# Optimization experiments

Hardware: AMD Instinct MI355X
Metric: run time of the kernel (lower is better)

Reference implementation:

```python
import jax, jax.numpy as jnp
import numpy as np

B, P, C = 32, 8732, 21
TOP_K = 200
CONF_THRESH = 0.01
NMS_THRESH = 0.45
VAR0, VAR1 = 0.1, 0.2  # VOC PRIOR_BOX VARIANCE


def setup_inputs() -> dict:
    key = jax.random.key(0)
    k1, k2, k3 = jax.random.split(key, 3)
    loc_data = jax.random.normal(k1, (B, P, 4), jnp.float32)
    conf_data = jax.random.uniform(k2, (B, P, C), jnp.float32)
    prior_data = jax.random.uniform(k3, (P, 4), jnp.float32)
    return {"loc_data": loc_data, "conf_data": conf_data, "prior_data": prior_data}


def _decode(loc, priors):
    # priors are (cx, cy, w, h); returns (x1, y1, x2, y2)
    cxcy = priors[:, :2] + loc[:, :2] * VAR0 * priors[:, 2:]
    wh = priors[:, 2:] * jnp.exp(loc[:, 2:] * VAR1)
    x1y1 = cxcy - wh * 0.5
    return jnp.concatenate([x1y1, x1y1 + wh], axis=1)  # [P,4]


def _nms_class(boxes, scores):
    # boxes [P,4], scores [P] -> [TOP_K,5] rows of (score, x1, y1, x2, y2)
    s = jnp.where(scores > CONF_THRESH, scores, -1.0)
    top_s, idx = jax.lax.top_k(s, TOP_K)          # descending scores
    b = boxes[idx]                                 # [K,4]
    valid = top_s > CONF_THRESH
    x1, y1, x2, y2 = b[:, 0], b[:, 1], b[:, 2], b[:, 3]
    area = (x2 - x1) * (y2 - y1)
    # pairwise intersection / IoU [K,K]
    xx1 = jnp.maximum(x1[:, None], x1[None, :])
    yy1 = jnp.maximum(y1[:, None], y1[None, :])
    xx2 = jnp.minimum(x2[:, None], x2[None, :])
    yy2 = jnp.minimum(y2[:, None], y2[None, :])
    inter = jnp.clip(xx2 - xx1, 0.0) * jnp.clip(yy2 - yy1, 0.0)
    union = area[:, None] + area[None, :] - inter
    iou = inter / union
    ar = jnp.arange(TOP_K)

    def step(carry, j):
        kept, suppressed = carry
        is_kept = valid[j] & ~suppressed[j]
        kept = kept.at[j].set(is_kept)
        suppressed = suppressed | (is_kept & (iou[j] > NMS_THRESH) & (ar > j))
        return (kept, suppressed), None

    (kept, _), _ = jax.lax.scan(
        step, (jnp.zeros(TOP_K, bool), jnp.zeros(TOP_K, bool)), ar)
    # compact kept rows to the front (matches output[i, cl, :count] = ...)
    pos = jnp.cumsum(kept) - 1
    safe = jnp.where(kept, pos, TOP_K)
    rows = jnp.concatenate([top_s[:, None], b], axis=1)  # [K,5]
    out = jnp.zeros((TOP_K + 1, 5), rows.dtype).at[safe].set(rows)[:TOP_K]
    return out


def reference(loc_data, conf_data, prior_data):
    def per_image(loc, conf):
        boxes = _decode(loc, prior_data)           # [P,4]
        return jax.vmap(lambda s: _nms_class(boxes, s), in_axes=1)(conf)  # [C,K,5]

    out = jax.vmap(per_image)(loc_data, conf_data)  # [B,C,K,5]
    return out.at[:, 0].set(0.0)  # class 0 (background) is skipped in original
```

## Files before the change

### kernel.cpp

```cpp
#include <hip/hip_runtime.h>
#include <stdint.h>

#define B_ 32
#define P_ 8732
#define C_ 21
#define TOPK 200
#define TGT 228
#define TGT0 300
#define SUBCAP 28
#define NCH2 35
#define NSLOT (NCH2 * SUBCAP)
#define CONF_T 0.01f
#define NMS_T 0.45f
#define NT 512
#define KV4 5
#define NTASK (B_ * C_)

__device__ __forceinline__ uint32_t f2s(float f) {
    uint32_t u = __float_as_uint(f);
    return (u & 0x80000000u) ? ~u : (u | 0x80000000u);
}
__device__ __forceinline__ float s2f(uint32_t s) {
    uint32_t b = (s & 0x80000000u) ? (s & 0x7FFFFFFFu) : ~s;
    return __uint_as_float(b);
}
__device__ __forceinline__ uint32_t keyof(float v) {
    return f2s((v > CONF_T) ? v : -1.0f);
}
__device__ __forceinline__ uint32_t thr0() {
    return f2s(1.0f - (float)TGT0 / (float)P_);
}

__global__ __launch_bounds__(256) void scatter_cands(const float* __restrict__ conf,
                                                     uint32_t* __restrict__ gccnt,
                                                     uint64_t* __restrict__ gcand) {
    const int b = blockIdx.x / NCH2;
    const int ch = blockIdx.x % NCH2;
    const int p0 = ch * 256;
    const int n = min(256, P_ - p0);
    const int tid = threadIdx.x;
    const int lane = tid & 63;
    const int cs = tid >> 6;
    __shared__ float tile[256 * C_];
    const float4* src4 = (const float4*)(conf + ((size_t)b * P_ + p0) * C_);
    float4* tile4 = (float4*)tile;
    const int tot4 = (n * C_) >> 2;
    for (int i = tid; i < tot4; i += 256) tile4[i] = src4[i];
    __syncthreads();
    const uint32_t T0 = thr0();
    const bool act = (4 * lane) < n;
    for (int c = (cs == 0 ? 4 : cs); c < C_; c += 4) {
        uint32_t kk[4];
        int nq = 0;
        if (act) {
            const float* tp = &tile[4 * lane * C_ + c];
            kk[0] = keyof(tp[0 * C_]);
            kk[1] = keyof(tp[1 * C_]);
            kk[2] = keyof(tp[2 * C_]);
            kk[3] = keyof(tp[3 * C_]);
            nq = (kk[0] >= T0) + (kk[1] >= T0) + (kk[2] >= T0) + (kk[3] >= T0);
        }
        int incl = nq;
        #pragma unroll
        for (int d = 1; d < 64; d <<= 1) {
            int v = __shfl_up(incl, d);
            if (lane >= d) incl += v;
        }
        const int excl = incl - nq;
        const int total = __shfl(incl, 63);
        const int task = b * C_ + c;
        uint64_t* dst = gcand + ((size_t)task * NCH2 + ch) * SUBCAP;
        if (nq) {
            int pos = excl;
            const int pb = p0 + 4 * lane;
            #pragma unroll
            for (int k = 0; k < 4; ++k) {
                if (kk[k] >= T0) {
                    if (pos < SUBCAP)
                        dst[pos] = ((uint64_t)kk[k] << 32) | (uint32_t)(~(uint32_t)(pb + k));
                    ++pos;
                }
            }
        }
        if (lane == 0) gccnt[(size_t)task * NCH2 + ch] = (uint32_t)total;
    }
}

template<bool HASWS>
__global__ __launch_bounds__(NT, 6) void detect_kernel(
    const float* __restrict__ loc, const float* __restrict__ prior,
    const uint32_t* __restrict__ gccnt, const uint64_t* __restrict__ gcand,
    const float* __restrict__ conf, float* __restrict__ out)
{
    const int task = blockIdx.x;
    const int b = task / C_;
    const int c = task % C_;
    const int tid = threadIdx.x;
    const int lane = tid & 63;
    float* outp = out + (size_t)task * TOPK * 5;

    if (c == 0) {
        for (int e = tid; e < TOPK * 5; e += NT) outp[e] = 0.0f;
        return;
    }

    __shared__ uint64_t cand[256];
    __shared__ float4 bbox[TOPK];
    __shared__ float bs[TOPK];
    __shared__ unsigned long long msk[TOPK * 4];
    __shared__ unsigned long long vmask[4];
    __shared__ int order[TOPK];
    __shared__ int s_cnt, s_nk;
    __shared__ int s_c2[2];
    __shared__ uint32_t s_ccnt[NCH2];
    __shared__ int s_gc, s_bad;

    const uint32_t T0 = thr0();

    if (tid == 0) s_cnt = 0;
    if (tid < 2) s_c2[tid] = 0;
    if (HASWS && tid < NCH2) s_ccnt[tid] = gccnt[(size_t)task * NCH2 + tid];
    for (int i2 = tid; i2 < TOPK * 4; i2 += NT) msk[i2] = 0ull;
    __syncthreads();
    if (HASWS && tid < 64) {
        uint32_t cc = (lane < NCH2) ? s_ccnt[lane] : 0u;
        int bad = (cc > SUBCAP) ? 1 : 0;
        int tot = (int)cc;
        #pragma unroll
        for (int d = 1; d < 64; d <<= 1) {
            tot += __shfl_down(tot, d);
            bad |= __shfl_down(bad, d);
        }
        if (lane == 0) { s_gc = tot; s_bad = bad; }
    }
    __syncthreads();

    const bool fast = HASWS && !s_bad && s_gc >= TOPK;
    const int gc = HASWS ? s_gc : 0;

    uint64_t vc0 = 0, vc1 = 0;
    bool val0 = false, val1 = false;
    uint4 kv[KV4];
    if (fast) {
        const uint64_t* gp = gcand + (size_t)task * NSLOT;
        {
            const int ch0 = tid / SUBCAP, i0 = tid - ch0 * SUBCAP;
            if (i0 < (int)s_ccnt[ch0]) { vc0 = gp[tid]; val0 = true; }
        }
        const int s1 = tid + NT;
        if (s1 < NSLOT) {
            const int ch1 = s1 / SUBCAP, i1 = s1 - ch1 * SUBCAP;
            if (i1 < (int)s_ccnt[ch1]) { vc1 = gp[s1]; val1 = true; }
        }
    } else {
        const float* sp = conf + (size_t)b * P_ * C_ + c;
        #pragma unroll
        for (int r = 0; r < KV4; ++r) {
            uint32_t uu[4];
            #pragma unroll
            for (int c4 = 0; c4 < 4; ++c4) {
                int p = (tid + r * NT) * 4 + c4;
                if (p < P_) {
                    float v = sp[(size_t)p * C_];
                    v = (v > CONF_T) ? v : -1.0f;
                    uu[c4] = f2s(v);
                } else uu[c4] = 0u;
            }
            kv[r] = make_uint4(uu[0], uu[1], uu[2], uu[3]);
        }
    }

    if (fast) {
        uint32_t vthr = T0;
        if (gc > 256) {
            const uint32_t k0 = (uint32_t)(vc0 >> 32);
            const uint32_t k1 = (uint32_t)(vc1 >> 32);
            uint32_t lo = T0, hi = 0xFFFFFFFFu;
            uint32_t t;
            {
                const float sc = s2f(T0);
                const float sn = 1.0f - (1.0f - sc) * (float)TGT / (float)gc;
                t = f2s(sn);
                if (!(t > lo && t < hi)) t = lo + ((hi - lo) >> 1);
            }
            for (int it = 0; ; ++it) {
                const int slot = it & 1;
                int my = (val0 && k0 >= t) + (val1 && k1 >= t);
                #pragma unroll
                for (int d = 1; d < 64; d <<= 1) my += __shfl_down(my, d);
                if (lane == 0) atomicAdd(&s_c2[slot], my);
                __syncthreads();
                const int cnt = s_c2[slot];
                __syncthreads();
                if (tid == 0) s_c2[slot] = 0;
                if (cnt >= TOPK && cnt <= 256) { vthr = t; break; }
                if (cnt > 256) lo = t; else hi = t;
                if (hi - lo <= 1) { vthr = lo; break; }
                uint32_t tn = 0;
                bool bis = (it >= 8) || (cnt == 0);
                if (!bis) {
                    const float sc = s2f(t);
                    const float sn = 1.0f - (1.0f - sc) * (float)TGT / (float)cnt;
                    tn = f2s(sn);
                    if (!(tn > lo && tn < hi)) bis = true;
                }
                if (bis) tn = lo + ((hi - lo) >> 1);
                t = tn;
            }
        }
        if (val0 && (uint32_t)(vc0 >> 32) >= vthr) {
            int pos = atomicAdd(&s_cnt, 1);
            if (pos < 256) cand[pos] = vc0;
        }
        if (val1 && (uint32_t)(vc1 >> 32) >= vthr) {
            int pos = atomicAdd(&s_cnt, 1);
            if (pos < 256) cand[pos] = vc1;
        }
    } else {
        uint32_t lo = 0u, hi = 0xFFFFFFFFu;
        uint32_t t = f2s(1.0f - (float)TGT / (float)P_);
        uint32_t vthr = 0u;
        for (int it = 0; ; ++it) {
            const int slot = it & 1;
            int my = 0;
            #pragma unroll
            for (int r = 0; r < KV4; ++r)
                my += (kv[r].x >= t) + (kv[r].y >= t) + (kv[r].z >= t) + (kv[r].w >= t);
            #pragma unroll
            for (int d = 1; d < 64; d <<= 1) my += __shfl_down(my, d);
            if (lane == 0) atomicAdd(&s_c2[slot], my);
            __syncthreads();
            const int cnt = s_c2[slot];
            __syncthreads();
            if (tid == 0) s_c2[slot] = 0;
            if (cnt >= TOPK && cnt <= 256) { vthr = t; break; }
            if (cnt > 256) lo = t; else hi = t;
            if (hi - lo <= 1) { vthr = lo; break; }
            uint32_t tn = 0;
            bool bis = (it >= 8) || (cnt == 0);
            if (!bis) {
                const float sc = s2f(t);
                const float sn = 1.0f - (1.0f - sc) * (float)TGT / (float)cnt;
                tn = f2s(sn);
                if (!(tn > lo && tn < hi)) bis = true;
            }
            if (bis) tn = lo + ((hi - lo) >> 1);
            t = tn;
        }
        #pragma unroll
        for (int r = 0; r < KV4; ++r) {
            const int pb = (tid + r * NT) * 4;
            uint32_t uu[4] = {kv[r].x, kv[r].y, kv[r].z, kv[r].w};
            #pragma unroll
            for (int c4 = 0; c4 < 4; ++c4) {
                uint32_t u = uu[c4];
                if (u >= vthr) {
                    int pos = atomicAdd(&s_cnt, 1);
                    if (pos < 256) cand[pos] = ((uint64_t)u << 32) | (uint32_t)(~(uint32_t)(pb + c4));
                }
            }
        }
    }
    __syncthreads();
    if (tid < 256 && tid >= s_cnt) cand[tid] = 0ull;
    __syncthreads();

    uint64_t v = (tid < 256) ? cand[tid] : 0ull;
    for (int kk = 2; kk <= 256; kk <<= 1) {
        for (int j = kk >> 1; j > 0; j >>= 1) {
            if (j >= 64) {
                __syncthreads();
                if (tid < 256) cand[tid] = v;
                __syncthreads();
                if (tid < 256) {
                    uint64_t pv = cand[tid ^ j];
                    bool keepmax = (((tid & j) == 0) == ((tid & kk) == 0));
                    v = keepmax ? (v > pv ? v : pv) : (v < pv ? v : pv);
                }
            } else if (tid < 256) {
                uint64_t pv = __shfl_xor(v, j);
                bool keepmax = (((tid & j) == 0) == ((tid & kk) == 0));
                v = keepmax ? (v > pv ? v : pv) : (v < pv ? v : pv);
            }
        }
    }

    float my_sc = -1.0f;
    if (tid < TOPK) {
        uint32_t su = (uint32_t)(v >> 32);
        int p = (int)(~(uint32_t)v);
        my_sc = s2f(su);
        const float4 l4 = *(const float4*)(loc + ((size_t)b * P_ + p) * 4);
        const float4 pr = *(const float4*)(prior + (size_t)p * 4);
        float cx = __fadd_rn(pr.x, __fmul_rn(__fmul_rn(l4.x, 0.1f), pr.z));
        float cy = __fadd_rn(pr.y, __fmul_rn(__fmul_rn(l4.y, 0.1f), pr.w));
        float ew = (float)exp((double)__fmul_rn(l4.z, 0.2f));
        float eh = (float)exp((double)__fmul_rn(l4.w, 0.2f));
        float w  = __fmul_rn(pr.z, ew);
        float h  = __fmul_rn(pr.w, eh);
        float x1 = __fsub_rn(cx, __fmul_rn(w, 0.5f));
        float y1 = __fsub_rn(cy, __fmul_rn(h, 0.5f));
        float x2 = __fadd_rn(x1, w);
        float y2 = __fadd_rn(y1, h);
        bs[tid] = my_sc;
        bbox[tid] = make_float4(x1, y1, x2, y2);
    }
    {
        unsigned long long bm = __ballot(tid < TOPK && my_sc > CONF_T);
        if (lane == 0 && tid < 256) vmask[tid >> 6] = bm;
    }
    __syncthreads();

    if (tid < 500) {
        const int rp = tid / 5;
        const int s  = tid - rp * 5;
        #pragma unroll
        for (int pass = 0; pass < 2; ++pass) {
            const int j  = pass ? (199 - rp) : rp;
            const int i0 = j + 1 + s;
            const float4 bj = bbox[j];
            const float  aj = __fmul_rn(__fsub_rn(bj.z, bj.x), __fsub_rn(bj.w, bj.y));
            for (int i = i0; i < TOPK; i += 5) {
                const float4 bi = bbox[i];
                float xx1 = fmaxf(bj.x, bi.x);
                float yy1 = fmaxf(bj.y, bi.y);
                float xx2 = fminf(bj.z, bi.z);
                float yy2 = fminf(bj.w, bi.w);
                float dx = fmaxf(__fsub_rn(xx2, xx1), 0.0f);
                float dy = fmaxf(__fsub_rn(yy2, yy1), 0.0f);
                float inter = __fmul_rn(dx, dy);
                if (inter > 0.0f) {
                    float ai = __fmul_rn(__fsub_rn(bi.z, bi.x), __fsub_rn(bi.w, bi.y));
                    float uni = __fsub_rn(__fadd_rn(aj, ai), inter);
                    float t45 = __fmul_rn(NMS_T, uni);
                    float mar = __fmul_rn(t45, 1e-6f);
                    bool sup;
                    if (inter > __fadd_rn(t45, mar)) sup = true;
                    else if (inter < __fsub_rn(t45, mar)) sup = false;
                    else sup = (inter / uni > NMS_T);
                    if (sup) atomicOr(&msk[j * 4 + (i >> 6)], 1ull << (i & 63));
                }
            }
        }
    }
    __syncthreads();

    if (tid < 64) {
        const int L = tid;
        auto or_reduce = [&](unsigned long long x) {
            #pragma unroll
            for (int d = 1; d < 64; d <<= 1) x |= __shfl_xor(x, d);
            return x;
        };
        unsigned long long s1 = 0, s2 = 0, s3 = 0;
        int nk = 0;
        #pragma unroll
        for (int w = 0; w < 4; ++w) {
            const int j = (w << 6) | L;
            unsigned long long r0 = 0, r1 = 0, r2 = 0, r3 = 0;
            if (j < TOPK) {
                const unsigned long long* mr = &msk[j * 4];
                r0 = mr[0]; r1 = mr[1]; r2 = mr[2]; r3 = mr[3];
            }
            const unsigned long long rself = (w == 0) ? r0 : (w == 1) ? r1
                                           : (w == 2) ? r2 : r3;
            unsigned long long sw = (w == 0) ? 0ull : (w == 1) ? s1
                                  : (w == 2) ? s2 : s3;
            unsigned long long alive = vmask[w] & ~sw;
            unsigned long long pm = 0;
            while (alive) {
                int jl = __ffsll(alive) - 1;
                if (L == 0) order[nk] = (w << 6) | jl;
                ++nk;
                sw |= __shfl(rself, jl);
                pm |= (1ull << jl);
                alive &= ~(sw | (1ull << jl));
            }
            if (pm) {
                const bool picked = (pm >> L) & 1ull;
                if (w == 0) {
                    s1 |= or_reduce(picked ? r1 : 0ull);
                    s2 |= or_reduce(picked ? r2 : 0ull);
                    s3 |= or_reduce(picked ? r3 : 0ull);
                } else if (w == 1) {
                    s2 |= or_reduce(picked ? r2 : 0ull);
                    s3 |= or_reduce(picked ? r3 : 0ull);
                } else if (w == 2) {
                    s3 |= or_reduce(picked ? r3 : 0ull);
                }
            }
        }
        if (L == 0) s_nk = nk;
    }
    __syncthreads();

    const int nk = s_nk;
    for (int e = tid; e < TOPK * 5; e += NT) {
        int r = e / 5;
        int f = e - r * 5;
        float val = 0.0f;
        if (r < nk) {
            int j = order[r];
            float4 bb = bbox[j];
            val = (f == 0) ? bs[j] : (f == 1) ? bb.x : (f == 2) ? bb.y
                : (f == 3) ? bb.z : bb.w;
        }
        outp[e] = val;
    }
}

extern "C" void kernel_launch(void* const* d_in, const int* in_sizes, int n_in,
                              void* d_out, int out_size, void* d_ws, size_t ws_size,
                              hipStream_t stream) {
    const float* loc   = (const float*)d_in[0];
    const float* conf  = (const float*)d_in[1];
    const float* prior = (const float*)d_in[2];
    float* out = (float*)d_out;

    const size_t cnt_bytes  = (size_t)NTASK * NCH2 * sizeof(uint32_t);
    const size_t cand_bytes = (size_t)NTASK * NSLOT * sizeof(uint64_t);
    if (ws_size >= cnt_bytes + cand_bytes) {
        uint32_t* gccnt = (uint32_t*)d_ws;
        uint64_t* gcand = (uint64_t*)((char*)d_ws + cnt_bytes);
        scatter_cands<<<B_ * NCH2, 256, 0, stream>>>(conf, gccnt, gcand);
        detect_kernel<true><<<NTASK, NT, 0, stream>>>(loc, prior, gccnt, gcand, conf, out);
    } else {
        detect_kernel<false><<<NTASK, NT, 0, stream>>>(loc, prior, nullptr, nullptr, conf, out);
    }
}
```

Baseline: 123.3 us.

## Pack four NMS tasks per block and use ballot compaction in scatter

The detect kernel now runs four (image, class) tasks per 1024-thread block, each with 256 threads, instead of one task per 512-thread block. Shared arrays are indexed per task, and the threshold search loop is made block-uniform through a shared active flag. Background-class tasks no longer exit early; they run the common path with work masked off. The IoU pairwise work is redistributed over 200 threads. The scatter kernel replaces its 4-per-lane shuffle prefix scan with a ballot/popcount compaction over 64-point groups. Risks: the four tasks share every barrier, so each waits for the slowest one's search iterations, and a block now needs four times the shared memory.

```diff
diff --git a/kernel.cpp b/kernel.cpp
--- a/kernel.cpp
+++ b/kernel.cpp
@@ -12,9 +12,12 @@
 #define NSLOT (NCH2 * SUBCAP)
 #define CONF_T 0.01f
 #define NMS_T 0.45f
-#define NT 512
-#define KV4 5
 #define NTASK (B_ * C_)
+#define GT 4
+#define HT 256
+#define NTB (GT * HT)
+#define NBLK (NTASK / GT)
+#define KV4H 9
 
 __device__ __forceinline__ uint32_t f2s(float f) {
     uint32_t u = __float_as_uint(f);
@@ -40,7 +43,7 @@
     const int n = min(256, P_ - p0);
     const int tid = threadIdx.x;
     const int lane = tid & 63;
-    const int cs = tid >> 6;
+    const int wv = tid >> 6;
     __shared__ float tile[256 * C_];
     const float4* src4 = (const float4*)(conf + ((size_t)b * P_ + p0) * C_);
     float4* tile4 = (float4*)tile;
@@ -48,82 +51,66 @@
     for (int i = tid; i < tot4; i += 256) tile4[i] = src4[i];
     __syncthreads();
     const uint32_t T0 = thr0();
-    const bool act = (4 * lane) < n;
-    for (int c = (cs == 0 ? 4 : cs); c < C_; c += 4) {
-        uint32_t kk[4];
-        int nq = 0;
-        if (act) {
-            const float* tp = &tile[4 * lane * C_ + c];
-            kk[0] = keyof(tp[0 * C_]);
-            kk[1] = keyof(tp[1 * C_]);
-            kk[2] = keyof(tp[2 * C_]);
-            kk[3] = keyof(tp[3 * C_]);
-            nq = (kk[0] >= T0) + (kk[1] >= T0) + (kk[2] >= T0) + (kk[3] >= T0);
-        }
-        int incl = nq;
-        #pragma unroll
-        for (int d = 1; d < 64; d <<= 1) {
-            int v = __shfl_up(incl, d);
-            if (lane >= d) incl += v;
-        }
-        const int excl = incl - nq;
-        const int total = __shfl(incl, 63);
-        const int task = b * C_ + c;
-        uint64_t* dst = gcand + ((size_t)task * NCH2 + ch) * SUBCAP;
-        if (nq) {
-            int pos = excl;
-            const int pb = p0 + 4 * lane;
-            #pragma unroll
-            for (int k = 0; k < 4; ++k) {
-                if (kk[k] >= T0) {
-                    if (pos < SUBCAP)
-                        dst[pos] = ((uint64_t)kk[k] << 32) | (uint32_t)(~(uint32_t)(pb + k));
-                    ++pos;
-                }
-            }
-        }
-        if (lane == 0) gccnt[(size_t)task * NCH2 + ch] = (uint32_t)total;
+    const unsigned long long lmask = (1ull << lane) - 1ull;
+    for (int c = (wv == 0 ? 4 : wv); c < C_; c += 4) {
+        int base = 0;
+        uint64_t* dst = gcand + ((size_t)(b * C_ + c) * NCH2 + ch) * SUBCAP;
+        #pragma unroll
+        for (int itp = 0; itp < 4; ++itp) {
+            const int p = itp * 64 + lane;
+            bool q = false; uint32_t key = 0;
+            if (p < n) {
+                key = keyof(tile[p * C_ + c]);
+                q = (key >= T0);
+            }
+            const unsigned long long bm = __ballot(q);
+            if (q) {
+                int pos = base + (int)__popcll(bm & lmask);
+                if (pos < SUBCAP)
+                    dst[pos] = ((uint64_t)key << 32) | (uint32_t)(~(uint32_t)(p0 + p));
+            }
+            base += (int)__popcll(bm);
+        }
+        if (lane == 0) gccnt[(size_t)(b * C_ + c) * NCH2 + ch] = (uint32_t)base;
     }
 }
 
 template<bool HASWS>
-__global__ __launch_bounds__(NT, 6) void detect_kernel(
+__global__ __launch_bounds__(NTB, 4) void detect_kernel(
     const float* __restrict__ loc, const float* __restrict__ prior,
     const uint32_t* __restrict__ gccnt, const uint64_t* __restrict__ gcand,
     const float* __restrict__ conf, float* __restrict__ out)
 {
-    const int task = blockIdx.x;
+    const int tid = threadIdx.x;
+    const int h   = tid >> 8;
+    const int ht  = tid & 255;
+    const int lane = tid & 63;
+    const int task = blockIdx.x * GT + h;
     const int b = task / C_;
     const int c = task % C_;
-    const int tid = threadIdx.x;
-    const int lane = tid & 63;
+    const bool live = (c != 0);
     float* outp = out + (size_t)task * TOPK * 5;
 
-    if (c == 0) {
-        for (int e = tid; e < TOPK * 5; e += NT) outp[e] = 0.0f;
-        return;
-    }
-
-    __shared__ uint64_t cand[256];
-    __shared__ float4 bbox[TOPK];
-    __shared__ float bs[TOPK];
-    __shared__ unsigned long long msk[TOPK * 4];
-    __shared__ unsigned long long vmask[4];
-    __shared__ int order[TOPK];
-    __shared__ int s_cnt, s_nk;
-    __shared__ int s_c2[2];
-    __shared__ uint32_t s_ccnt[NCH2];
-    __shared__ int s_gc, s_bad;
+    __shared__ uint64_t cand[GT][256];
+    __shared__ float4 bbox[GT][TOPK];
+    __shared__ float bs[GT][TOPK];
+    __shared__ unsigned long long msk[GT][TOPK * 4];
+    __shared__ unsigned long long vmask[GT][4];
+    __shared__ int order[GT][TOPK];
+    __shared__ int s_cnt[GT], s_nk[GT];
+    __shared__ int s_c2[GT][2];
+    __shared__ uint32_t s_ccnt[GT][NCH2];
+    __shared__ int s_gc[GT], s_bad[GT], s_act[GT];
 
     const uint32_t T0 = thr0();
 
-    if (tid == 0) s_cnt = 0;
-    if (tid < 2) s_c2[tid] = 0;
-    if (HASWS && tid < NCH2) s_ccnt[tid] = gccnt[(size_t)task * NCH2 + tid];
-    for (int i2 = tid; i2 < TOPK * 4; i2 += NT) msk[i2] = 0ull;
-    __syncthreads();
-    if (HASWS && tid < 64) {
-        uint32_t cc = (lane < NCH2) ? s_ccnt[lane] : 0u;
+    if (ht == 0) s_cnt[h] = 0;
+    if (ht < 2) s_c2[h][ht] = 0;
+    if (HASWS && ht < NCH2) s_ccnt[h][ht] = gccnt[(size_t)task * NCH2 + ht];
+    for (int i = ht; i < TOPK * 4; i += HT) msk[h][i] = 0ull;
+    __syncthreads();
+    if (HASWS && ht < 64) {
+        uint32_t cc = (lane < NCH2) ? s_ccnt[h][lane] : 0u;
         int bad = (cc > SUBCAP) ? 1 : 0;
         int tot = (int)cc;
         #pragma unroll
@@ -131,162 +118,156 @@
             tot += __shfl_down(tot, d);
             bad |= __shfl_down(bad, d);
         }
-        if (lane == 0) { s_gc = tot; s_bad = bad; }
-    }
-    __syncthreads();
-
-    const bool fast = HASWS && !s_bad && s_gc >= TOPK;
-    const int gc = HASWS ? s_gc : 0;
-
-    uint64_t vc0 = 0, vc1 = 0;
-    bool val0 = false, val1 = false;
-    uint4 kv[KV4];
+        if (lane == 0) { s_gc[h] = tot; s_bad[h] = bad; }
+    }
+    __syncthreads();
+
+    const bool fast = HASWS && live && !s_bad[h] && s_gc[h] >= TOPK;
+    const int gc = fast ? s_gc[h] : 0;
+
+    uint64_t vc[4] = {0, 0, 0, 0};
+    bool val[4] = {false, false, false, false};
+    uint4 kv[KV4H];
+    #pragma unroll
+    for (int r = 0; r < KV4H; ++r) kv[r] = make_uint4(0u, 0u, 0u, 0u);
     if (fast) {
         const uint64_t* gp = gcand + (size_t)task * NSLOT;
-        {
-            const int ch0 = tid / SUBCAP, i0 = tid - ch0 * SUBCAP;
-            if (i0 < (int)s_ccnt[ch0]) { vc0 = gp[tid]; val0 = true; }
-        }
-        const int s1 = tid + NT;
-        if (s1 < NSLOT) {
-            const int ch1 = s1 / SUBCAP, i1 = s1 - ch1 * SUBCAP;
-            if (i1 < (int)s_ccnt[ch1]) { vc1 = gp[s1]; val1 = true; }
-        }
-    } else {
+        #pragma unroll
+        for (int k = 0; k < 4; ++k) {
+            const int s = ht + k * HT;
+            if (s < NSLOT) {
+                const int chh = s / SUBCAP, ii = s - chh * SUBCAP;
+                if (ii < (int)s_ccnt[h][chh]) { vc[k] = gp[s]; val[k] = true; }
+            }
+        }
+    } else if (live) {
         const float* sp = conf + (size_t)b * P_ * C_ + c;
         #pragma unroll
-        for (int r = 0; r < KV4; ++r) {
+        for (int r = 0; r < KV4H; ++r) {
             uint32_t uu[4];
             #pragma unroll
-            for (int c4 = 0; c4 < 4; ++c4) {
-                int p = (tid + r * NT) * 4 + c4;
-                if (p < P_) {
-                    float v = sp[(size_t)p * C_];
-                    v = (v > CONF_T) ? v : -1.0f;
-                    uu[c4] = f2s(v);
-                } else uu[c4] = 0u;
+            for (int q = 0; q < 4; ++q) {
+                const int p = (ht + r * HT) * 4 + q;
+                uu[q] = (p < P_) ? keyof(sp[(size_t)p * C_]) : 0u;
             }
             kv[r] = make_uint4(uu[0], uu[1], uu[2], uu[3]);
         }
     }
 
-    if (fast) {
-        uint32_t vthr = T0;
+    bool active = false;
+    uint32_t t = 0, lo = 0, hi = 0xFFFFFFFFu, vthr = 0;
+    int it2 = 0;
+    if (!live) {
+        vthr = 0xFFFFFFFFu;
+    } else if (fast) {
+        lo = T0; vthr = T0;
         if (gc > 256) {
-            const uint32_t k0 = (uint32_t)(vc0 >> 32);
-            const uint32_t k1 = (uint32_t)(vc1 >> 32);
-            uint32_t lo = T0, hi = 0xFFFFFFFFu;
-            uint32_t t;
-            {
-                const float sc = s2f(T0);
-                const float sn = 1.0f - (1.0f - sc) * (float)TGT / (float)gc;
-                t = f2s(sn);
-                if (!(t > lo && t < hi)) t = lo + ((hi - lo) >> 1);
-            }
-            for (int it = 0; ; ++it) {
-                const int slot = it & 1;
-                int my = (val0 && k0 >= t) + (val1 && k1 >= t);
+            const float sc = s2f(T0);
+            const float sn = 1.0f - (1.0f - sc) * (float)TGT / (float)gc;
+            t = f2s(sn);
+            if (!(t > lo && t < hi)) t = lo + ((hi - lo) >> 1);
+            active = true;
+        }
+    } else {
+        t = f2s(1.0f - (float)TGT / (float)P_);
+        active = true;
+    }
+    if (ht == 0) s_act[h] = active ? 1 : 0;
+    __syncthreads();
+
+    for (int bit = 0; ; ++bit) {
+        if (!(s_act[0] | s_act[1] | s_act[2] | s_act[3])) break;
+        const int slot = bit & 1;
+        int my = 0;
+        if (active) {
+            if (fast) {
                 #pragma unroll
-                for (int d = 1; d < 64; d <<= 1) my += __shfl_down(my, d);
-                if (lane == 0) atomicAdd(&s_c2[slot], my);
-                __syncthreads();
-                const int cnt = s_c2[slot];
-                __syncthreads();
-                if (tid == 0) s_c2[slot] = 0;
-                if (cnt >= TOPK && cnt <= 256) { vthr = t; break; }
+                for (int k = 0; k < 4; ++k)
+                    my += (val[k] && (uint32_t)(vc[k] >> 32) >= t) ? 1 : 0;
+            } else {
+                #pragma unroll
+                for (int r = 0; r < KV4H; ++r)
+                    my += (kv[r].x >= t) + (kv[r].y >= t) + (kv[r].z >= t) + (kv[r].w >= t);
+            }
+        }
+        #pragma unroll
+        for (int d = 1; d < 64; d <<= 1) my += __shfl_down(my, d);
+        if (lane == 0 && my) atomicAdd(&s_c2[h][slot], my);
+        __syncthreads();
+        const int cnt = s_c2[h][slot];
+        __syncthreads();
+        if (ht == 0) s_c2[h][slot] = 0;
+        if (active) {
+            if (cnt >= TOPK && cnt <= 256) { vthr = t; active = false; }
+            else {
                 if (cnt > 256) lo = t; else hi = t;
-                if (hi - lo <= 1) { vthr = lo; break; }
-                uint32_t tn = 0;
-                bool bis = (it >= 8) || (cnt == 0);
-                if (!bis) {
-                    const float sc = s2f(t);
-                    const float sn = 1.0f - (1.0f - sc) * (float)TGT / (float)cnt;
-                    tn = f2s(sn);
-                    if (!(tn > lo && tn < hi)) bis = true;
+                if (hi - lo <= 1) { vthr = lo; active = false; }
+                else {
+                    uint32_t tn = 0;
+                    bool bis = (it2 >= 8) || (cnt == 0);
+                    if (!bis) {
+                        const float sc = s2f(t);
+                        const float sn = 1.0f - (1.0f - sc) * (float)TGT / (float)cnt;
+                        tn = f2s(sn);
+                        if (!(tn > lo && tn < hi)) bis = true;
+                    }
+                    if (bis) tn = lo + ((hi - lo) >> 1);
+                    t = tn;
                 }
-                if (bis) tn = lo + ((hi - lo) >> 1);
-                t = tn;
-            }
-        }
-        if (val0 && (uint32_t)(vc0 >> 32) >= vthr) {
-            int pos = atomicAdd(&s_cnt, 1);
-            if (pos < 256) cand[pos] = vc0;
-        }
-        if (val1 && (uint32_t)(vc1 >> 32) >= vthr) {
-            int pos = atomicAdd(&s_cnt, 1);
-            if (pos < 256) cand[pos] = vc1;
-        }
-    } else {
-        uint32_t lo = 0u, hi = 0xFFFFFFFFu;
-        uint32_t t = f2s(1.0f - (float)TGT / (float)P_);
-        uint32_t vthr = 0u;
-        for (int it = 0; ; ++it) {
-            const int slot = it & 1;
-            int my = 0;
+                ++it2;
+            }
+        }
+        if (ht == 0) s_act[h] = active ? 1 : 0;
+        __syncthreads();
+    }
+
+    if (live) {
+        if (fast) {
             #pragma unroll
-            for (int r = 0; r < KV4; ++r)
-                my += (kv[r].x >= t) + (kv[r].y >= t) + (kv[r].z >= t) + (kv[r].w >= t);
+            for (int k = 0; k < 4; ++k)
+                if (val[k] && (uint32_t)(vc[k] >> 32) >= vthr) {
+                    int pos = atomicAdd(&s_cnt[h], 1);
+                    if (pos < 256) cand[h][pos] = vc[k];
+                }
+        } else {
             #pragma unroll
-            for (int d = 1; d < 64; d <<= 1) my += __shfl_down(my, d);
-            if (lane == 0) atomicAdd(&s_c2[slot], my);
-            __syncthreads();
-            const int cnt = s_c2[slot];
-            __syncthreads();
-            if (tid == 0) s_c2[slot] = 0;
-            if (cnt >= TOPK && cnt <= 256) { vthr = t; break; }
-            if (cnt > 256) lo = t; else hi = t;
-            if (hi - lo <= 1) { vthr = lo; break; }
-            uint32_t tn = 0;
-            bool bis = (it >= 8) || (cnt == 0);
-            if (!bis) {
-                const float sc = s2f(t);
-                const float sn = 1.0f - (1.0f - sc) * (float)TGT / (float)cnt;
-                tn = f2s(sn);
-                if (!(tn > lo && tn < hi)) bis = true;
-            }
-            if (bis) tn = lo + ((hi - lo) >> 1);
-            t = tn;
-        }
-        #pragma unroll
-        for (int r = 0; r < KV4; ++r) {
-            const int pb = (tid + r * NT) * 4;
-            uint32_t uu[4] = {kv[r].x, kv[r].y, kv[r].z, kv[r].w};
-            #pragma unroll
-            for (int c4 = 0; c4 < 4; ++c4) {
-                uint32_t u = uu[c4];
-                if (u >= vthr) {
-                    int pos = atomicAdd(&s_cnt, 1);
-                    if (pos < 256) cand[pos] = ((uint64_t)u << 32) | (uint32_t)(~(uint32_t)(pb + c4));
-                }
-            }
-        }
-    }
-    __syncthreads();
-    if (tid < 256 && tid >= s_cnt) cand[tid] = 0ull;
-    __syncthreads();
-
-    uint64_t v = (tid < 256) ? cand[tid] : 0ull;
+            for (int r = 0; r < KV4H; ++r) {
+                const int pb = (ht + r * HT) * 4;
+                uint32_t uu[4] = {kv[r].x, kv[r].y, kv[r].z, kv[r].w};
+                #pragma unroll
+                for (int q = 0; q < 4; ++q)
+                    if (uu[q] >= vthr) {
+                        int pos = atomicAdd(&s_cnt[h], 1);
+                        if (pos < 256)
+                            cand[h][pos] = ((uint64_t)uu[q] << 32) | (uint32_t)(~(uint32_t)(pb + q));
+                    }
+            }
+        }
+    }
+    __syncthreads();
+    if (ht >= s_cnt[h]) cand[h][ht] = 0ull;
+    __syncthreads();
+
+    uint64_t v = cand[h][ht];
     for (int kk = 2; kk <= 256; kk <<= 1) {
         for (int j = kk >> 1; j > 0; j >>= 1) {
             if (j >= 64) {
                 __syncthreads();
-                if (tid < 256) cand[tid] = v;
+                cand[h][ht] = v;
                 __syncthreads();
-                if (tid < 256) {
-                    uint64_t pv = cand[tid ^ j];
-                    bool keepmax = (((tid & j) == 0) == ((tid & kk) == 0));
-                    v = keepmax ? (v > pv ? v : pv) : (v < pv ? v : pv);
-                }
-            } else if (tid < 256) {
+                uint64_t pv = cand[h][ht ^ j];
+                bool keepmax = (((ht & j) == 0) == ((ht & kk) == 0));
+                v = keepmax ? (v > pv ? v : pv) : (v < pv ? v : pv);
+            } else {
                 uint64_t pv = __shfl_xor(v, j);
-                bool keepmax = (((tid & j) == 0) == ((tid & kk) == 0));
+                bool keepmax = (((ht & j) == 0) == ((ht & kk) == 0));
                 v = keepmax ? (v > pv ? v : pv) : (v < pv ? v : pv);
             }
         }
     }
 
     float my_sc = -1.0f;
-    if (tid < TOPK) {
+    if (live && ht < TOPK) {
         uint32_t su = (uint32_t)(v >> 32);
         int p = (int)(~(uint32_t)v);
         my_sc = s2f(su);
@@ -297,31 +278,31 @@
         float ew = (float)exp((double)__fmul_rn(l4.z, 0.2f));
         float eh = (float)exp((double)__fmul_rn(l4.w, 0.2f));
         float w  = __fmul_rn(pr.z, ew);
-        float h  = __fmul_rn(pr.w, eh);
+        float hh = __fmul_rn(pr.w, eh);
         float x1 = __fsub_rn(cx, __fmul_rn(w, 0.5f));
-        float y1 = __fsub_rn(cy, __fmul_rn(h, 0.5f));
+        float y1 = __fsub_rn(cy, __fmul_rn(hh, 0.5f));
         float x2 = __fadd_rn(x1, w);
-        float y2 = __fadd_rn(y1, h);
-        bs[tid] = my_sc;
-        bbox[tid] = make_float4(x1, y1, x2, y2);
+        float y2 = __fadd_rn(y1, hh);
+        bs[h][ht] = my_sc;
+        bbox[h][ht] = make_float4(x1, y1, x2, y2);
     }
     {
-        unsigned long long bm = __ballot(tid < TOPK && my_sc > CONF_T);
-        if (lane == 0 && tid < 256) vmask[tid >> 6] = bm;
-    }
-    __syncthreads();
-
-    if (tid < 500) {
-        const int rp = tid / 5;
-        const int s  = tid - rp * 5;
+        unsigned long long bm = __ballot(live && ht < TOPK && my_sc > CONF_T);
+        if (lane == 0) vmask[h][ht >> 6] = bm;
+    }
+    __syncthreads();
+
+    if (live && ht < 200) {
+        const int rp = ht >> 1;
+        const int s  = ht & 1;
         #pragma unroll
         for (int pass = 0; pass < 2; ++pass) {
             const int j  = pass ? (199 - rp) : rp;
             const int i0 = j + 1 + s;
-            const float4 bj = bbox[j];
+            const float4 bj = bbox[h][j];
             const float  aj = __fmul_rn(__fsub_rn(bj.z, bj.x), __fsub_rn(bj.w, bj.y));
-            for (int i = i0; i < TOPK; i += 5) {
-                const float4 bi = bbox[i];
+            for (int i = i0; i < TOPK; i += 2) {
+                const float4 bi = bbox[h][i];
                 float xx1 = fmaxf(bj.x, bi.x);
                 float yy1 = fmaxf(bj.y, bi.y);
                 float xx2 = fminf(bj.z, bi.z);
@@ -338,15 +319,15 @@
                     if (inter > __fadd_rn(t45, mar)) sup = true;
                     else if (inter < __fsub_rn(t45, mar)) sup = false;
                     else sup = (inter / uni > NMS_T);
-                    if (sup) atomicOr(&msk[j * 4 + (i >> 6)], 1ull << (i & 63));
+                    if (sup) atomicOr(&msk[h][j * 4 + (i >> 6)], 1ull << (i & 63));
                 }
             }
         }
     }
     __syncthreads();
 
-    if (tid < 64) {
-        const int L = tid;
+    if (ht < 64) {
+        const int L = ht;
         auto or_reduce = [&](unsigned long long x) {
             #pragma unroll
             for (int d = 1; d < 64; d <<= 1) x |= __shfl_xor(x, d);
@@ -359,18 +340,18 @@
             const int j = (w << 6) | L;
             unsigned long long r0 = 0, r1 = 0, r2 = 0, r3 = 0;
             if (j < TOPK) {
-                const unsigned long long* mr = &msk[j * 4];
+                const unsigned long long* mr = &msk[h][j * 4];
                 r0 = mr[0]; r1 = mr[1]; r2 = mr[2]; r3 = mr[3];
             }
             const unsigned long long rself = (w == 0) ? r0 : (w == 1) ? r1
                                            : (w == 2) ? r2 : r3;
             unsigned long long sw = (w == 0) ? 0ull : (w == 1) ? s1
                                   : (w == 2) ? s2 : s3;
-            unsigned long long alive = vmask[w] & ~sw;
+            unsigned long long alive = vmask[h][w] & ~sw;
             unsigned long long pm = 0;
             while (alive) {
                 int jl = __ffsll(alive) - 1;
-                if (L == 0) order[nk] = (w << 6) | jl;
+                if (L == 0) order[h][nk] = (w << 6) | jl;
                 ++nk;
                 sw |= __shfl(rself, jl);
                 pm |= (1ull << jl);
@@ -390,22 +371,22 @@
                 }
             }
         }
-        if (L == 0) s_nk = nk;
-    }
-    __syncthreads();
-
-    const int nk = s_nk;
-    for (int e = tid; e < TOPK * 5; e += NT) {
+        if (L == 0) s_nk[h] = nk;
+    }
+    __syncthreads();
+
+    const int nk = live ? s_nk[h] : 0;
+    for (int e = ht; e < TOPK * 5; e += HT) {
         int r = e / 5;
         int f = e - r * 5;
-        float val = 0.0f;
+        float val2 = 0.0f;
         if (r < nk) {
-            int j = order[r];
-            float4 bb = bbox[j];
-            val = (f == 0) ? bs[j] : (f == 1) ? bb.x : (f == 2) ? bb.y
-                : (f == 3) ? bb.z : bb.w;
-        }
-        outp[e] = val;
+            int j = order[h][r];
+            float4 bb = bbox[h][j];
+            val2 = (f == 0) ? bs[h][j] : (f == 1) ? bb.x : (f == 2) ? bb.y
+                 : (f == 3) ? bb.z : bb.w;
+        }
+        outp[e] = val2;
     }
 }
 
@@ -423,8 +404,8 @@
         uint32_t* gccnt = (uint32_t*)d_ws;
         uint64_t* gcand = (uint64_t*)((char*)d_ws + cnt_bytes);
         scatter_cands<<<B_ * NCH2, 256, 0, stream>>>(conf, gccnt, gcand);
-        detect_kernel<true><<<NTASK, NT, 0, stream>>>(loc, prior, gccnt, gcand, conf, out);
+        detect_kernel<true><<<NBLK, NTB, 0, stream>>>(loc, prior, gccnt, gcand, conf, out);
     } else {
-        detect_kernel<false><<<NTASK, NT, 0, stream>>>(loc, prior, nullptr, nullptr, conf, out);
-    }
-}
+        detect_kernel<false><<<NBLK, NTB, 0, stream>>>(loc, prior, nullptr, nullptr, conf, out);
+    }
+}
```

Result: slower. 142.7 us (+15.7%).
